# Kernel tuning notes

Measured on AMD Instinct MI355X. Metric: run time of the kernel, lower is better.

Reference implementation:

```python
import jax, jax.numpy as jnp
import numpy as np

B, T, H, S, NH = 8, 4096, 1024, 64, 16
DH = H // NH
L = T // S  # tokens per sentence (contiguous partition)


def setup_inputs() -> dict:
    key = jax.random.key(0)
    ks = jax.random.split(key, 10)
    init = lambda k, shape: (jax.random.normal(k, shape, dtype=jnp.float32) * 0.02)
    starts = jnp.arange(S, dtype=jnp.int32) * L
    bounds = jnp.stack([starts, starts + L], axis=-1)  # [S,2]
    sentence_boundaries = jnp.broadcast_to(bounds, (B, S, 2))
    return {
        "context_hidden": jax.random.normal(ks[0], (B, T, H), dtype=jnp.float32),
        "sentence_boundaries": sentence_boundaries,
        "in_proj_w": init(ks[1], (3 * H, H)),
        "in_proj_b": jnp.zeros((3 * H,), jnp.float32),
        "out_w": init(ks[2], (H, H)),
        "out_b": jnp.zeros((H,), jnp.float32),
        "w1": init(ks[3], (H, 2 * H)),
        "b1": jnp.zeros((H,), jnp.float32),
        "w2": init(ks[4], (1, H)),
        "b2": jnp.zeros((1,), jnp.float32),
    }


def _forward(h, sentence_boundaries, in_proj_w, in_proj_b, out_w, out_b, w1, b1, w2, b2):
    starts = sentence_boundaries[:, :, 0]  # [B,S]
    ends = sentence_boundaries[:, :, 1]    # [B,S]
    t = jnp.arange(T, dtype=jnp.int32)
    # membership: token t belongs to sentence s iff start <= t < end
    member = (t[None, :, None] >= starts[:, None, :]) & (t[None, :, None] < ends[:, None, :])  # [B,T,S]
    mf = member.astype(h.dtype)
    counts = jnp.clip(mf.sum(axis=1), 1.0)  # [B,S]
    # segment mean pooling (encode_sentences)
    sent_repr = jnp.einsum('bts,bth->bsh', mf, h) / counts[..., None]  # [B,S,H]

    # multihead self-attention over sentence reprs (eval mode, no dropout)
    qkv = sent_repr @ in_proj_w.T + in_proj_b  # [B,S,3H]
    q, k, v = jnp.split(qkv, 3, axis=-1)
    q = q.reshape(B, S, NH, DH)
    k = k.reshape(B, S, NH, DH)
    v = v.reshape(B, S, NH, DH)
    scores = jnp.einsum('bqhd,bkhd->bhqk', q, k) / jnp.sqrt(jnp.asarray(DH, h.dtype))
    attn = jax.nn.softmax(scores, axis=-1)
    ctx = jnp.einsum('bhqk,bkhd->bqhd', attn, v).reshape(B, S, H)
    attended = ctx @ out_w.T + out_b  # [B,S,H]

    # gather each token's sentence repr
    sid = jnp.clip(member.astype(jnp.int32).argmax(axis=-1), 0, S - 1)  # [B,T]
    covered = member.any(axis=-1)  # [B,T]
    att_tok = jnp.take_along_axis(attended, sid[..., None], axis=1)  # [B,T,H]

    # coherence scorer MLP on concat([token, sent_repr]) without materializing concat
    hid = jax.nn.relu(h @ w1[:, :H].T + att_tok @ w1[:, H:].T + b1)  # [B,T,H]
    score = (hid @ w2.T + b2)[..., 0]  # [B,T]
    score = jnp.where(covered, score, 0.0)
    return h + score[..., None] * h


def reference(context_hidden, sentence_boundaries, in_proj_w, in_proj_b, out_w, out_b, w1, b1, w2, b2):
    return _forward(context_hidden, sentence_boundaries, in_proj_w, in_proj_b,
                    out_w, out_b, w1, b1, w2, b2)
```

## Files before the change

### kernel.cpp

```cpp
#include <hip/hip_runtime.h>
#include <stdint.h>

#define BB 8
#define TT 4096
#define HH 1024
#define SS 64
#define NHH 16
#define DHH 64

typedef __attribute__((ext_vector_type(8))) short short8;
typedef __attribute__((ext_vector_type(8))) unsigned short ushortx8;
typedef __attribute__((ext_vector_type(4))) float f32x4;
typedef unsigned short u16;

#define GLOAD16(gp, lp)                                                   \
  __builtin_amdgcn_global_load_lds(                                      \
      (const __attribute__((address_space(1))) void*)(gp),               \
      (__attribute__((address_space(3))) void*)(lp), 16, 0, 0)

__device__ __forceinline__ u16 f2bf(float f) {
  union { float f; uint32_t u; } v;
  v.f = f;
  uint32_t u = v.u;
  uint32_t r = u + 0x7fffu + ((u >> 16) & 1u);
  return (u16)(r >> 16);
}

__device__ __forceinline__ float bf2f(u16 b) {
  union { uint32_t u; float f; } v;
  v.u = ((uint32_t)b) << 16;
  return v.f;
}

__device__ __forceinline__ void stage_tile(u16* lds, const float* src, int ld, int tid) {
#pragma unroll
  for (int q = 0; q < 4; ++q) {
    int slot_id = tid + (q << 8);
    int row = slot_id >> 3;
    int sl = slot_id & 7;
    const float* p = src + (size_t)row * ld + (sl << 3);
    float4 x0 = *(const float4*)(p);
    float4 x1 = *(const float4*)(p + 4);
    ushortx8 o;
    o[0] = f2bf(x0.x); o[1] = f2bf(x0.y); o[2] = f2bf(x0.z); o[3] = f2bf(x0.w);
    o[4] = f2bf(x1.x); o[5] = f2bf(x1.y); o[6] = f2bf(x1.z); o[7] = f2bf(x1.w);
    *(ushortx8*)(&lds[(row << 6) + (((sl ^ (row & 7)) << 3))]) = o;
  }
}

__global__ __launch_bounds__(256) void conv_tile_kernel(const float* __restrict__ src,
                                                        int ld, int ntile_k,
                                                        u16* __restrict__ dst) {
  int bid = blockIdx.x;
  int rt = bid / ntile_k;
  int kt = bid - rt * ntile_k;
  const float* s0 = src + (size_t)rt * 128 * ld + kt * 64;
  u16* d0 = dst + (size_t)bid * 8192;
  int tid = threadIdx.x;
#pragma unroll
  for (int q = 0; q < 4; ++q) {
    int slot_id = tid + (q << 8);
    int row = slot_id >> 3;
    int sl = slot_id & 7;
    const float* p = s0 + (size_t)row * ld + (sl << 3);
    float4 x0 = *(const float4*)(p);
    float4 x1 = *(const float4*)(p + 4);
    ushortx8 o;
    o[0] = f2bf(x0.x); o[1] = f2bf(x0.y); o[2] = f2bf(x0.z); o[3] = f2bf(x0.w);
    o[4] = f2bf(x1.x); o[5] = f2bf(x1.y); o[6] = f2bf(x1.z); o[7] = f2bf(x1.w);
    *(ushortx8*)(&d0[(row << 6) + (((sl ^ (row & 7)) << 3))]) = o;
  }
}

__global__ __launch_bounds__(256) void pool_bf_kernel(const u16* __restrict__ hbf,
                                                      const int* __restrict__ bounds,
                                                      float* __restrict__ sent) {
  int bs = blockIdx.x;
  int b = bs >> 6;
  int start = bounds[bs * 2];
  int end = bounds[bs * 2 + 1];
  int lo = max(start, 0), hi = min(end, TT);
  int cnt = max(hi - lo, 0);
  float inv = 1.0f / (float)max(cnt, 1);
  int tid = threadIdx.x;
  int sg = tid >> 1;
  int half = tid & 1;
  int kt = sg >> 3, slot = sg & 7;
  float a[8] = {};
  for (int t = lo + half; t < hi; t += 2) {
    int grow = b * TT + t;
    int rt = grow >> 7, r = grow & 127;
    const u16* tile = hbf + ((size_t)rt * 16 + kt) * 8192;
    ushortx8 v = *(const ushortx8*)(&tile[(r << 6) + ((slot ^ (r & 7)) << 3)]);
#pragma unroll
    for (int j = 0; j < 8; ++j) a[j] += bf2f(v[j]);
  }
#pragma unroll
  for (int j = 0; j < 8; ++j) a[j] += __shfl_xor(a[j], 1);
  if (half == 0) {
    float* d = sent + (size_t)bs * HH + sg * 8;
#pragma unroll
    for (int j = 0; j < 8; ++j) d[j] = a[j] * inv;
  }
}

__global__ __launch_bounds__(256) void setup_misc(const float* __restrict__ ipb,
                                                  const float* __restrict__ outb,
                                                  const float* __restrict__ b1,
                                                  const int* __restrict__ bounds,
                                                  float* __restrict__ qkv,
                                                  float* __restrict__ att,
                                                  float* __restrict__ cbuf,
                                                  int* __restrict__ sid) {
  int idx = blockIdx.x * 256 + threadIdx.x;
  const int STR = 2048 * 256;
  for (int i = idx; i < 512 * 3072; i += STR) qkv[i] = ipb[i % 3072];
  for (int i = idx; i < 512 * 1024; i += STR) att[i] = outb[i & 1023];
  for (int i = idx; i < 512 * 1024; i += STR) cbuf[i] = b1[i & 1023];
  if (idx < BB * TT) {
    int b = idx >> 12, t = idx & (TT - 1);
    int r = -1;
    for (int s = 0; s < SS; ++s) {
      int st = bounds[(b * SS + s) * 2], en = bounds[(b * SS + s) * 2 + 1];
      if (t >= st && t < en) { r = s; break; }
    }
    sid[idx] = r;
  }
}

__global__ __launch_bounds__(256) void gemm_bt_atomic(const float* __restrict__ A, int lda,
                                                      const float* __restrict__ Bm, int ldb,
                                                      float* __restrict__ C, int ldc,
                                                      int kper) {
  __shared__ u16 As[128 * 64];
  __shared__ u16 Bs[128 * 64];
  int tid = threadIdx.x;
  int m0 = blockIdx.x * 128, n0 = blockIdx.y * 128;
  int kbeg = blockIdx.z * kper;
  f32x4 acc[4][4] = {};

  for (int k0 = kbeg; k0 < kbeg + kper; k0 += 64) {
    __syncthreads();
    stage_tile(As, A + (size_t)m0 * lda + k0, lda, tid);
    stage_tile(Bs, Bm + (size_t)n0 * ldb + k0, ldb, tid);
    __syncthreads();
    int lane = tid & 63, wid = tid >> 6;
    int wm = wid >> 1, wn = wid & 1;
    int lr = lane & 15, lg = lane >> 4;
#pragma unroll
    for (int kk = 0; kk < 2; ++kk) {
      short8 af[4], bfr[4];
#pragma unroll
      for (int i = 0; i < 4; ++i) {
        int arow = wm * 64 + i * 16 + lr;
        int aslot = (kk * 4 + lg) ^ (arow & 7);
        af[i] = *(const short8*)(&As[(arow << 6) + (aslot << 3)]);
        int brow = wn * 64 + i * 16 + lr;
        int bslot = (kk * 4 + lg) ^ (brow & 7);
        bfr[i] = *(const short8*)(&Bs[(brow << 6) + (bslot << 3)]);
      }
#pragma unroll
      for (int i = 0; i < 4; ++i)
#pragma unroll
        for (int j = 0; j < 4; ++j)
          acc[i][j] = __builtin_amdgcn_mfma_f32_16x16x32_bf16(af[i], bfr[j], acc[i][j], 0, 0, 0);
    }
  }

  int lane = tid & 63, wid = tid >> 6;
  int wm = wid >> 1, wn = wid & 1;
  int lr = lane & 15, lg = lane >> 4;
#pragma unroll
  for (int i = 0; i < 4; ++i)
#pragma unroll
    for (int j = 0; j < 4; ++j)
#pragma unroll
      for (int r = 0; r < 4; ++r) {
        int row = m0 + wm * 64 + i * 16 + lg * 4 + r;
        int col = n0 + wn * 64 + j * 16 + lr;
        atomicAdd(&C[(size_t)row * ldc + col], acc[i][j][r]);
      }
}

__global__ __launch_bounds__(256) void attn_kernel(const float* __restrict__ qkv,
                                                   float* __restrict__ ctx) {
  int bh = blockIdx.x;
  int b = bh >> 4, nh = bh & 15;
  __shared__ float q[64][64], k[64][64], v[64][64], s[64][64];
  int tid = threadIdx.x;
  const float* base = qkv + (size_t)b * SS * 3072 + nh * 64;
  for (int e = tid; e < 4096; e += 256) {
    int i = e >> 6, d = e & 63;
    q[i][d] = base[(size_t)i * 3072 + d];
    k[i][d] = base[(size_t)i * 3072 + 1024 + d];
    v[i][d] = base[(size_t)i * 3072 + 2048 + d];
  }
  __syncthreads();
  for (int e = tid; e < 4096; e += 256) {
    int i = e >> 6, j = e & 63;
    float acc = 0.f;
#pragma unroll 8
    for (int d = 0; d < 64; ++d) acc += q[i][d] * k[j][d];
    s[i][j] = acc * 0.125f;
  }
  __syncthreads();
  {
    int r = tid >> 2, sub = tid & 3;
    int j0 = sub * 16;
    float m = -1e30f;
#pragma unroll
    for (int j = 0; j < 16; ++j) m = fmaxf(m, s[r][j0 + j]);
    m = fmaxf(m, __shfl_xor(m, 1));
    m = fmaxf(m, __shfl_xor(m, 2));
    float sum = 0.f;
#pragma unroll
    for (int j = 0; j < 16; ++j) {
      float e_ = __expf(s[r][j0 + j] - m);
      s[r][j0 + j] = e_;
      sum += e_;
    }
    sum += __shfl_xor(sum, 1);
    sum += __shfl_xor(sum, 2);
    float inv = 1.0f / sum;
#pragma unroll
    for (int j = 0; j < 16; ++j) s[r][j0 + j] *= inv;
  }
  __syncthreads();
  for (int e = tid; e < 4096; e += 256) {
    int i = e >> 6, d = e & 63;
    float acc = 0.f;
#pragma unroll 8
    for (int j = 0; j < 64; ++j) acc += s[i][j] * v[j][d];
    ctx[((size_t)b * SS + i) * HH + nh * 64 + d] = acc;
  }
}

__global__ __launch_bounds__(256) void score_partial(const u16* __restrict__ hbf,
                                                     const u16* __restrict__ wbf,
                                                     const float* __restrict__ cbuf,
                                                     const float* __restrict__ w2,
                                                     const int* __restrict__ sid_arr,
                                                     float* __restrict__ score_part) {
  __shared__ u16 As[8192];
  __shared__ u16 Bs[8192];
  __shared__ float w2_lds[128];
  __shared__ int sid_lds[128];
  __shared__ float red[128];

  int tid = threadIdx.x;
  int bid = blockIdx.x;
  int x = bid & 7;
  int g = bid >> 3;
  int mt = x * 32 + (g >> 3);
  int c = g & 7;
  int n0 = c * 128;
  size_t g0 = (size_t)mt * 128;
  int b = (int)(g0 >> 12);
  const u16* asrc = hbf + (size_t)mt * 16 * 8192;
  const u16* bsrc = wbf + (size_t)c * 16 * 8192;

  if (tid < 128) {
    w2_lds[tid] = w2[n0 + tid];
    sid_lds[tid] = sid_arr[g0 + tid];
    red[tid] = 0.f;
  }

  int lane = tid & 63, wid = tid >> 6;
  int wv = wid, ln = lane;
  int wm = wid >> 1, wn = wid & 1;
  int lr = lane & 15, lg = lane >> 4;

  f32x4 acc[4][4] = {};
  for (int kt = 0; kt < 16; ++kt) {
    __syncthreads();
    const u16* at = asrc + kt * 8192;
    const u16* bt = bsrc + kt * 8192;
#pragma unroll
    for (int q = 0; q < 4; ++q) {
      int off = q * 2048 + wv * 512 + ln * 8;
      GLOAD16(at + off, &As[q * 2048 + wv * 512]);
      GLOAD16(bt + off, &Bs[q * 2048 + wv * 512]);
    }
    __syncthreads();
#pragma unroll
    for (int kk = 0; kk < 2; ++kk) {
      short8 af[4], bfr[4];
#pragma unroll
      for (int i = 0; i < 4; ++i) {
        int arow = wm * 64 + i * 16 + lr;
        int aslot = (kk * 4 + lg) ^ (arow & 7);
        af[i] = *(const short8*)(&As[(arow << 6) + (aslot << 3)]);
        int brow = wn * 64 + i * 16 + lr;
        int bslot = (kk * 4 + lg) ^ (brow & 7);
        bfr[i] = *(const short8*)(&Bs[(brow << 6) + (bslot << 3)]);
      }
#pragma unroll
      for (int i = 0; i < 4; ++i)
#pragma unroll
        for (int j = 0; j < 4; ++j)
          acc[i][j] = __builtin_amdgcn_mfma_f32_16x16x32_bf16(af[i], bfr[j], acc[i][j], 0, 0, 0);
    }
  }

  float sp[4][4];
#pragma unroll
  for (int i = 0; i < 4; ++i) {
#pragma unroll
    for (int r = 0; r < 4; ++r) {
      int rowl = wm * 64 + i * 16 + lg * 4 + r;
      int s = sid_lds[rowl];
      int sc = s < 0 ? 0 : s;
      const float* crow = cbuf + ((size_t)b * SS + sc) * HH + n0;
      float accs = 0.f;
#pragma unroll
      for (int j = 0; j < 4; ++j) {
        int coll = wn * 64 + j * 16 + lr;
        float t = acc[i][j][r] + crow[coll];
        if (t > 0.f) accs += t * w2_lds[coll];
      }
      sp[i][r] = accs;
    }
  }

#pragma unroll
  for (int i = 0; i < 4; ++i)
#pragma unroll
    for (int r = 0; r < 4; ++r) {
      float v = sp[i][r];
      v += __shfl_xor(v, 1);
      v += __shfl_xor(v, 2);
      v += __shfl_xor(v, 4);
      v += __shfl_xor(v, 8);
      sp[i][r] = v;
    }
  if (lr == 0) {
#pragma unroll
    for (int i = 0; i < 4; ++i)
#pragma unroll
      for (int r = 0; r < 4; ++r)
        atomicAdd(&red[wm * 64 + i * 16 + lg * 4 + r], sp[i][r]);
  }
  __syncthreads();
  if (tid < 128) score_part[(size_t)c * (BB * TT) + g0 + tid] = red[tid];
}

__global__ __launch_bounds__(256) void scale_kernel(const float* __restrict__ h,
                                                    const float* __restrict__ score_part,
                                                    const float* __restrict__ b2,
                                                    const int* __restrict__ sid_arr,
                                                    float* __restrict__ out) {
  __shared__ float fac[16];
  int tid = threadIdx.x;
  int r0 = blockIdx.x * 16;
  if (tid < 16) {
    int t = r0 + tid;
    float s = b2[0];
#pragma unroll
    for (int c = 0; c < 8; ++c) s += score_part[(size_t)c * (BB * TT) + t];
    fac[tid] = (sid_arr[t] >= 0) ? (1.0f + s) : 1.0f;
  }
  __syncthreads();
  const float4* h4 = (const float4*)h + (size_t)r0 * 256;
  float4* o4 = (float4*)out + (size_t)r0 * 256;
  for (int e = tid; e < 16 * 256; e += 256) {
    float f = fac[e >> 8];
    float4 v = h4[e];
    v.x *= f; v.y *= f; v.z *= f; v.w *= f;
    o4[e] = v;
  }
}

extern "C" void kernel_launch(void* const* d_in, const int* in_sizes, int n_in,
                              void* d_out, int out_size, void* d_ws, size_t ws_size,
                              hipStream_t stream) {
  const float* h        = (const float*)d_in[0];
  const int*   bounds   = (const int*)d_in[1];
  const float* in_proj_w = (const float*)d_in[2];
  const float* in_proj_b = (const float*)d_in[3];
  const float* out_w    = (const float*)d_in[4];
  const float* out_b    = (const float*)d_in[5];
  const float* w1       = (const float*)d_in[6];
  const float* b1       = (const float*)d_in[7];
  const float* w2       = (const float*)d_in[8];
  const float* b2       = (const float*)d_in[9];
  float* out = (float*)d_out;

  char* ws = (char*)d_ws;
  float* sent  = (float*)(ws);
  float* qkv   = (float*)(ws + (2ull << 20));
  float* ctx   = (float*)(ws + (8ull << 20));
  float* att   = (float*)(ws + (10ull << 20));
  float* cbuf  = (float*)(ws + (12ull << 20));
  int*   sid   = (int*)(ws + (14ull << 20));
  float* spart = (float*)(ws + (15ull << 20));
  u16*   hbf   = (u16*)(ws + (16ull << 20));
  u16*   wbf   = (u16*)(ws + (80ull << 20));

  conv_tile_kernel<<<256 * 16, 256, 0, stream>>>(h, HH, 16, hbf);
  conv_tile_kernel<<<8 * 16, 256, 0, stream>>>(w1, 2 * HH, 16, wbf);

  pool_bf_kernel<<<BB * SS, 256, 0, stream>>>(hbf, bounds, sent);
  setup_misc<<<2048, 256, 0, stream>>>(in_proj_b, out_b, b1, bounds, qkv, att, cbuf, sid);

  gemm_bt_atomic<<<dim3(4, 24, 4), 256, 0, stream>>>(sent, HH, in_proj_w, HH, qkv, 3 * HH, 256);
  attn_kernel<<<BB * NHH, 256, 0, stream>>>(qkv, ctx);
  gemm_bt_atomic<<<dim3(4, 8, 4), 256, 0, stream>>>(ctx, HH, out_w, HH, att, HH, 256);
  gemm_bt_atomic<<<dim3(4, 8, 4), 256, 0, stream>>>(att, HH, w1 + HH, 2 * HH, cbuf, HH, 256);

  score_partial<<<2048, 256, 0, stream>>>(hbf, wbf, cbuf, w2, sid, spart);
  scale_kernel<<<2048, 256, 0, stream>>>(h, spart, b2, sid, out);
}
```

Measured before the change: 326.1 us.

## Multi-buffer LDS tiles in score GEMM with two-stage prefetch pipeline

Replaces the single-buffered LDS staging in the score_partial GEMM with a 4-slot ring buffer. Global-to-LDS loads for k-tile i+2 are issued before computing tile i, with explicit vmcnt waits and one barrier per iteration instead of two. This aims to hide global load latency behind MFMA work. In exchange, LDS use rises from 32KB to 128KB of tiles per block, which may reduce occupancy or exceed the LDS limit on some configurations.

```diff
diff --git a/kernel.cpp b/kernel.cpp
--- a/kernel.cpp
+++ b/kernel.cpp
@@ -17,6 +17,10 @@
   __builtin_amdgcn_global_load_lds(                                      \
       (const __attribute__((address_space(1))) void*)(gp),               \
       (__attribute__((address_space(3))) void*)(lp), 16, 0, 0)
+
+#define WAITVM(n)                                                         \
+  asm volatile("s_waitcnt vmcnt(" #n ")" ::: "memory");                  \
+  __builtin_amdgcn_sched_barrier(0)
 
 __device__ __forceinline__ u16 f2bf(float f) {
   union { float f; uint32_t u; } v;
@@ -241,8 +245,8 @@
                                                      const float* __restrict__ w2,
                                                      const int* __restrict__ sid_arr,
                                                      float* __restrict__ score_part) {
-  __shared__ u16 As[8192];
-  __shared__ u16 Bs[8192];
+  __shared__ u16 Abuf[4][8192];
+  __shared__ u16 Bbuf[4][8192];
   __shared__ float w2_lds[128];
   __shared__ int sid_lds[128];
   __shared__ float red[128];
@@ -265,42 +269,58 @@
     red[tid] = 0.f;
   }
 
-  int lane = tid & 63, wid = tid >> 6;
-  int wv = wid, ln = lane;
-  int wm = wid >> 1, wn = wid & 1;
+  int lane = tid & 63, wv = tid >> 6;
+  int wm = wv >> 1, wn = wv & 1;
   int lr = lane & 15, lg = lane >> 4;
 
+#define STAGE_KT(kt, bufi)                                                \
+  {                                                                       \
+    const u16* at_ = asrc + (kt) * 8192;                                  \
+    const u16* bt_ = bsrc + (kt) * 8192;                                  \
+    _Pragma("unroll")                                                     \
+    for (int q = 0; q < 4; ++q) {                                         \
+      int off_ = q * 2048 + wv * 512 + lane * 8;                          \
+      GLOAD16(at_ + off_, &Abuf[bufi][q * 2048 + wv * 512]);              \
+      GLOAD16(bt_ + off_, &Bbuf[bufi][q * 2048 + wv * 512]);              \
+    }                                                                     \
+  }
+
+  STAGE_KT(0, 0);
+  STAGE_KT(1, 1);
+
   f32x4 acc[4][4] = {};
-  for (int kt = 0; kt < 16; ++kt) {
-    __syncthreads();
-    const u16* at = asrc + kt * 8192;
-    const u16* bt = bsrc + kt * 8192;
-#pragma unroll
-    for (int q = 0; q < 4; ++q) {
-      int off = q * 2048 + wv * 512 + ln * 8;
-      GLOAD16(at + off, &As[q * 2048 + wv * 512]);
-      GLOAD16(bt + off, &Bs[q * 2048 + wv * 512]);
-    }
-    __syncthreads();
+  for (int i = 0; i < 16; ++i) {
+    if (i < 14) {
+      STAGE_KT(i + 2, (i + 2) & 3);
+      WAITVM(16);
+    } else if (i == 14) {
+      WAITVM(8);
+    } else {
+      WAITVM(0);
+    }
+    __builtin_amdgcn_s_barrier();
+    const u16* As = Abuf[i & 3];
+    const u16* Bs = Bbuf[i & 3];
 #pragma unroll
     for (int kk = 0; kk < 2; ++kk) {
       short8 af[4], bfr[4];
 #pragma unroll
-      for (int i = 0; i < 4; ++i) {
-        int arow = wm * 64 + i * 16 + lr;
+      for (int ii = 0; ii < 4; ++ii) {
+        int arow = wm * 64 + ii * 16 + lr;
         int aslot = (kk * 4 + lg) ^ (arow & 7);
-        af[i] = *(const short8*)(&As[(arow << 6) + (aslot << 3)]);
-        int brow = wn * 64 + i * 16 + lr;
+        af[ii] = *(const short8*)(&As[(arow << 6) + (aslot << 3)]);
+        int brow = wn * 64 + ii * 16 + lr;
         int bslot = (kk * 4 + lg) ^ (brow & 7);
-        bfr[i] = *(const short8*)(&Bs[(brow << 6) + (bslot << 3)]);
+        bfr[ii] = *(const short8*)(&Bs[(brow << 6) + (bslot << 3)]);
       }
 #pragma unroll
-      for (int i = 0; i < 4; ++i)
+      for (int ii = 0; ii < 4; ++ii)
 #pragma unroll
         for (int j = 0; j < 4; ++j)
-          acc[i][j] = __builtin_amdgcn_mfma_f32_16x16x32_bf16(af[i], bfr[j], acc[i][j], 0, 0, 0);
-    }
-  }
+          acc[ii][j] = __builtin_amdgcn_mfma_f32_16x16x32_bf16(af[ii], bfr[j], acc[ii][j], 0, 0, 0);
+    }
+  }
+#undef STAGE_KT
 
   float sp[4][4];
 #pragma unroll
```

Result: slower. 381.8 us (+17.1%).
